# Optimization experiments

Measured on AMD Instinct MI355X. Metric: run time of the kernel, lower is better.

Reference implementation:

```python
import jax, jax.numpy as jnp
import numpy as np
from jax import lax

PART = 224   # PART_IMAGE_SIZE
PAD = 224    # PAD_SIZE
TOPN = 4
IOU_THRESH = 0.25
N_ANCHORS = 1614


def _conv(x, w, b, stride, pad):
    y = lax.conv_general_dilated(x, w, (stride, stride), [(pad, pad), (pad, pad)],
                                 dimension_numbers=('NCHW', 'OIHW', 'NCHW'))
    return y + b[None, :, None, None]


def _iou(box, boxes):
    # box [4], boxes [N,4] as (y0,x0,y1,x1)
    yy0 = jnp.maximum(box[0], boxes[:, 0]); xx0 = jnp.maximum(box[1], boxes[:, 1])
    yy1 = jnp.minimum(box[2], boxes[:, 2]); xx1 = jnp.minimum(box[3], boxes[:, 3])
    inter = jnp.clip(yy1 - yy0, 0.0) * jnp.clip(xx1 - xx0, 0.0)
    a = (box[2] - box[0]) * (box[3] - box[1])
    areas = (boxes[:, 2] - boxes[:, 0]) * (boxes[:, 3] - boxes[:, 1])
    return inter / (a + areas - inter)


def _nms(scores, boxes):
    # hard NMS keeping TOPN boxes; returns indices [TOPN]
    valid = jnp.ones(scores.shape, dtype=bool)
    idxs = []
    for _ in range(TOPN):
        i = jnp.argmax(jnp.where(valid, scores, -jnp.inf))
        idxs.append(i)
        valid = valid & (_iou(boxes[i], boxes) <= IOU_THRESH)
    return jnp.stack(idxs)


def _crop_resize(img, box):
    # img [3,Hp,Wp] padded image, box [4] float; bilinear, align_corners=True,
    # matching F.interpolate(x_pad[:, :, y0:y1, x0:x1], (PART, PART))
    Hp, Wp = img.shape[1], img.shape[2]
    def coords(c0, c1, L):
        t = jnp.arange(PART, dtype=img.dtype) / (PART - 1)
        c = c0 + (c1 - 1.0 - c0) * t          # absolute source coordinate
        cf = jnp.floor(c)
        lo = jnp.clip(cf.astype(jnp.int32), 0, L - 1)
        hi = jnp.clip(lo + 1, 0, L - 1)
        return lo, hi, c - cf
    yl, yh, wy = coords(box[0], box[2], Hp)
    xl, xh, wx = coords(box[1], box[3], Wp)
    g = lambda yi, xi: img[:, yi[:, None], xi[None, :]]   # [3,PART,PART]
    return ((1 - wy)[:, None] * ((1 - wx) * g(yl, xl) + wx * g(yl, xh))
            + wy[:, None] * ((1 - wx) * g(yh, xl) + wx * g(yh, xh)))


def setup_inputs() -> dict:
    key = jax.random.key(0)
    ks = jax.random.split(key, 20)
    x = jax.random.uniform(ks[0], (16, 3, 448, 448), dtype=jnp.float32)
    rpn_feature = jax.random.normal(ks[1], (16, 2048, 14, 14), dtype=jnp.float32)
    # valid boxes inside the padded 896x896 image
    y0 = jax.random.randint(ks[2], (N_ANCHORS,), 0, 560)
    x0 = jax.random.randint(ks[3], (N_ANCHORS,), 0, 560)
    h = jax.random.randint(ks[4], (N_ANCHORS,), 32, 336)
    w = jax.random.randint(ks[5], (N_ANCHORS,), 32, 336)
    anchors = jnp.stack([y0, x0, jnp.minimum(y0 + h, 896), jnp.minimum(x0 + w, 896)], axis=1).astype(jnp.int32)
    s = 0.02
    inp = {
        'x': x, 'rpn_feature': rpn_feature, 'anchors': anchors,
        'w_down1': jax.random.normal(ks[6], (128, 2048, 3, 3), jnp.float32) * s,
        'b_down1': jnp.zeros((128,), jnp.float32),
        'w_down2': jax.random.normal(ks[7], (128, 128, 3, 3), jnp.float32) * s,
        'b_down2': jnp.zeros((128,), jnp.float32),
        'w_down3': jax.random.normal(ks[8], (128, 128, 3, 3), jnp.float32) * s,
        'b_down3': jnp.zeros((128,), jnp.float32),
        'w_tidy1': jax.random.normal(ks[9], (6, 128, 1, 1), jnp.float32) * s,
        'b_tidy1': jnp.zeros((6,), jnp.float32),
        'w_tidy2': jax.random.normal(ks[10], (6, 128, 1, 1), jnp.float32) * s,
        'b_tidy2': jnp.zeros((6,), jnp.float32),
        'w_tidy3': jax.random.normal(ks[11], (9, 128, 1, 1), jnp.float32) * s,
        'b_tidy3': jnp.zeros((9,), jnp.float32),
    }
    return inp


def reference(x, rpn_feature, anchors,
              w_down1, b_down1, w_down2, b_down2, w_down3, b_down3,
              w_tidy1, b_tidy1, w_tidy2, b_tidy2, w_tidy3, b_tidy3):
    B = x.shape[0]
    # ProposalNet
    d1 = jax.nn.relu(_conv(rpn_feature, w_down1, b_down1, 1, 1))   # [B,128,14,14]
    d2 = jax.nn.relu(_conv(d1, w_down2, b_down2, 2, 1))            # [B,128,7,7]
    d3 = jax.nn.relu(_conv(d2, w_down3, b_down3, 2, 1))            # [B,128,4,4]
    t1 = _conv(d1, w_tidy1, b_tidy1, 1, 0).reshape(B, -1)
    t2 = _conv(d2, w_tidy2, b_tidy2, 1, 0).reshape(B, -1)
    t3 = _conv(d3, w_tidy3, b_tidy3, 1, 0).reshape(B, -1)
    rpn_score = jnp.concatenate([t1, t2, t3], axis=1)              # [B, 1614]
    boxes = anchors.astype(x.dtype)                                # [N,4]
    top_n_index = jax.vmap(lambda s: _nms(s, boxes))(rpn_score)    # [B,TOPN]
    top_n_prob = jnp.take_along_axis(rpn_score, top_n_index, axis=1)
    x_pad = jnp.pad(x, ((0, 0), (0, 0), (PAD, PAD), (PAD, PAD)))   # [B,3,896,896]
    sel_boxes = boxes[top_n_index]                                 # [B,TOPN,4]
    part_imgs = jax.vmap(lambda img, bxs: jax.vmap(lambda b: _crop_resize(img, b))(bxs))(x_pad, sel_boxes)
    # part_imgs: [B,TOPN,3,PART,PART]
    return rpn_score, top_n_index, top_n_prob, part_imgs
```

## Files before the change

kernel.cpp:

```cpp
#include <hip/hip_runtime.h>
#include <hip/hip_bf16.h>

#define NB 16
#define NA 1614

typedef __bf16 bf16x8 __attribute__((ext_vector_type(8)));
typedef float f32x4 __attribute__((ext_vector_type(4)));

__device__ __forceinline__ unsigned short f2bf(float v) {
  unsigned u = __float_as_uint(v);
  unsigned r = (u + 0x7FFFu + ((u >> 16) & 1u)) >> 16;
  return (unsigned short)r;
}
__device__ __forceinline__ float bf2f(unsigned short s) {
  return __uint_as_float(((unsigned)s) << 16);
}

__global__ void prep_w(const float* __restrict__ w, unsigned short* __restrict__ wTh,
                       unsigned short* __restrict__ wTl) {
  int e = blockIdx.x * 256 + threadIdx.x;
  if (e >= 9 * 128 * 2048) return;
  int tap = e / (128 * 2048);
  int rem = e - tap * (128 * 2048);
  int oc = rem >> 11, ic = rem & 2047;
  float v = w[((size_t)oc * 2048 + ic) * 9 + tap];
  unsigned short h = f2bf(v);
  wTh[e] = h;
  wTl[e] = f2bf(v - bf2f(h));
}

__global__ __launch_bounds__(256, 3)
void conv1_mfma(const float* __restrict__ in, const unsigned short* __restrict__ wTh,
                const unsigned short* __restrict__ wTl, float* __restrict__ pout,
                int atomic_mode) {
  const int bid = blockIdx.x;
  const int b  = bid & 15;
  const int nh = (bid >> 4) & 1;
  const int kc = bid >> 5;
  const int tid = threadIdx.x;
  const int wid = tid >> 6, lane = tid & 63;
  const int wm = wid & 1, wn = wid >> 1;
  const int q = lane >> 4, ln = lane & 15;

  __shared__ unsigned short sAh[256 * 40];
  __shared__ unsigned short sAl[256 * 40];
  __shared__ unsigned short sBh[64 * 40];
  __shared__ unsigned short sBl[64 * 40];

  for (int e = tid; e < 5120; e += 256) {
    ((unsigned int*)sAh)[e] = 0u;
    ((unsigned int*)sAl)[e] = 0u;
  }

  int abase[7];
#pragma unroll
  for (int mf = 0; mf < 7; mf++) {
    int row = wm * 112 + mf * 16 + ln;
    int y = row / 14, x = row - y * 14;
    abase[mf] = ((row < 196) ? (y * 16 + x) : 0) * 40 + q * 8;
  }

  f32x4 acc[7][2];
#pragma unroll
  for (int mf = 0; mf < 7; mf++)
#pragma unroll
    for (int nf = 0; nf < 2; nf++) acc[mf][nf] = (f32x4){0.f, 0.f, 0.f, 0.f};

  const float* inb = in + (size_t)b * 2048 * 196;

  const int boc = tid >> 2, bic0 = (tid & 3) * 8;
  const size_t bocbase = (size_t)(nh * 64 + boc) << 11;

  uint4 pvh, pvl;
  {
    size_t g = bocbase + kc * 128 + bic0;
    pvh = *(const uint4*)(wTh + g);
    pvl = *(const uint4*)(wTl + g);
  }

  for (int it = 0; it < 36; it++) {
    const int ks = it / 9, tap = it - ks * 9;
    const int icg0 = kc * 128 + ks * 32;
    __syncthreads();
    *(uint4*)(sBh + boc * 40 + bic0) = pvh;
    *(uint4*)(sBl + boc * 40 + bic0) = pvl;
    if (tap == 0) {
#pragma unroll
      for (int r = 0; r < 25; r++) {
        int e = tid + 256 * r;
        if (e < 6272) {
          int icl = e & 31, posl = e >> 5;
          float v = inb[(size_t)(icg0 + icl) * 196 + posl];
          unsigned short h = f2bf(v);
          unsigned short l = f2bf(v - bf2f(h));
          int py = posl / 14, px = posl - py * 14;
          int ad = ((py + 1) * 16 + px + 1) * 40 + icl;
          sAh[ad] = h;
          sAl[ad] = l;
        }
      }
    }
    {
      const int nit = (it < 35) ? it + 1 : 35;
      const int ks2 = nit / 9, tap2 = nit - ks2 * 9;
      size_t g = (size_t)tap2 * (128 * 2048) + bocbase + kc * 128 + ks2 * 32 + bic0;
      pvh = *(const uint4*)(wTh + g);
      pvl = *(const uint4*)(wTl + g);
    }
    __syncthreads();

    const int t40 = ((tap / 3) * 16 + (tap % 3)) * 40;
    bf16x8 bh[2], bl[2];
#pragma unroll
    for (int nf = 0; nf < 2; nf++) {
      const int bb = (wn * 32 + nf * 16 + ln) * 40 + q * 8;
      bh[nf] = *(const bf16x8*)(sBh + bb);
      bl[nf] = *(const bf16x8*)(sBl + bb);
    }
#pragma unroll
    for (int mf = 0; mf < 7; mf++) {
      bf16x8 ah = *(const bf16x8*)(sAh + abase[mf] + t40);
      bf16x8 al = *(const bf16x8*)(sAl + abase[mf] + t40);
#pragma unroll
      for (int nf = 0; nf < 2; nf++) {
        acc[mf][nf] = __builtin_amdgcn_mfma_f32_16x16x32_bf16(ah, bh[nf], acc[mf][nf], 0, 0, 0);
        acc[mf][nf] = __builtin_amdgcn_mfma_f32_16x16x32_bf16(al, bh[nf], acc[mf][nf], 0, 0, 0);
        acc[mf][nf] = __builtin_amdgcn_mfma_f32_16x16x32_bf16(ah, bl[nf], acc[mf][nf], 0, 0, 0);
      }
    }
  }

  if (atomic_mode) {
#pragma unroll
    for (int mf = 0; mf < 7; mf++) {
      const int row0 = wm * 112 + mf * 16 + q * 4;
#pragma unroll
      for (int nf = 0; nf < 2; nf++) {
        const int oc = nh * 64 + wn * 32 + nf * 16 + ln;
        float* dst = pout + ((size_t)b * 128 + oc) * 196;
#pragma unroll
        for (int r = 0; r < 4; r++) {
          const int row = row0 + r;
          if (row < 196) atomicAdd(dst + row, acc[mf][nf][r]);
        }
      }
    }
  } else {
    float* pk = pout + ((size_t)kc * NB + b) * 196 * 128;
#pragma unroll
    for (int mf = 0; mf < 7; mf++) {
      const int row0 = wm * 112 + mf * 16 + q * 4;
#pragma unroll
      for (int nf = 0; nf < 2; nf++) {
        const int oc = nh * 64 + wn * 32 + nf * 16 + ln;
#pragma unroll
        for (int r = 0; r < 4; r++) {
          const int row = row0 + r;
          if (row < 196) pk[(size_t)row * 128 + oc] = acc[mf][nf][r];
        }
      }
    }
  }
}

__global__ void conv1_finish_p(const float* __restrict__ p1, const float* __restrict__ bias,
                               float* __restrict__ d1) {
  const int i = blockIdx.x * 256 + threadIdx.x;
  if (i >= NB * 196 * 128) return;
  const int oc = i & 127;
  const int t = i >> 7;
  const int pos = t % 196, b = t / 196;
  float s = bias[oc];
#pragma unroll
  for (int k = 0; k < 16; k++) s += p1[(size_t)k * (NB * 196 * 128) + i];
  d1[((size_t)b * 128 + oc) * 196 + pos] = fmaxf(s, 0.f);
}

__global__ void conv1_finish_a(float* __restrict__ d1, const float* __restrict__ bias) {
  const int i = blockIdx.x * 256 + threadIdx.x;
  if (i >= NB * 128 * 196) return;
  const int oc = (i / 196) & 127;
  d1[i] = fmaxf(d1[i] + bias[oc], 0.f);
}

__global__ void conv2_part(const float* __restrict__ d1, const float* __restrict__ w,
                           float* __restrict__ p2) {
  const int bid = blockIdx.x;
  const int kc = bid & 3, oct = (bid >> 2) & 3, b = bid >> 4;
  const int ic0 = kc * 32, oc0 = oct * 32;
  const int tid = threadIdx.x;
  const int ocl = tid >> 3, rw = tid & 7;

  __shared__ float s_in[32 * 320];
  __shared__ float s_w[32 * 324];

#pragma unroll
  for (int r = 0; r < 32; r++) {
    const int e = tid + 256 * r;
    const int ch = e >> 8, idx = e & 255;
    const int tr = idx >> 4, tc = idx & 15;
    const int iy = tr - 1, ix = tc - 1;
    float v = 0.f;
    if ((unsigned)iy < 14u && (unsigned)ix < 14u)
      v = d1[((size_t)b * 128 + ic0 + ch) * 196 + iy * 14 + ix];
    s_in[ch * 320 + tr * 20 + tc] = v;
  }
#pragma unroll
  for (int r = 0; r < 36; r++) {
    const int e = tid + 256 * r;
    const int oc = e / 288, rem = e - oc * 288;
    const int ch = rem / 9, tap = rem - ch * 9;
    s_w[ch * 324 + tap * 36 + oc] =
        w[(size_t)(oc0 + oc) * 1152 + (size_t)ic0 * 9 + rem];
  }
  __syncthreads();

  if (rw < 7) {
    float acc[7] = {};
    for (int ic = 0; ic < 32; ic++) {
      const float* wrow = s_w + ic * 324 + ocl;
      const float* irow = s_in + ic * 320;
#pragma unroll
      for (int ky = 0; ky < 3; ky++) {
        const float* r = irow + (2 * rw + ky) * 20;
        const float4 f0 = *(const float4*)(r);
        const float4 f1 = *(const float4*)(r + 4);
        const float4 f2 = *(const float4*)(r + 8);
        const float4 f3 = *(const float4*)(r + 12);
        const float ev[8] = {f0.x, f0.z, f1.x, f1.z, f2.x, f2.z, f3.x, f3.z};
        const float od[7] = {f0.y, f0.w, f1.y, f1.w, f2.y, f2.w, f3.y};
        const float w0 = wrow[(ky * 3 + 0) * 36];
        const float w1 = wrow[(ky * 3 + 1) * 36];
        const float w2 = wrow[(ky * 3 + 2) * 36];
#pragma unroll
        for (int x = 0; x < 7; x++)
          acc[x] = fmaf(w0, ev[x], fmaf(w1, od[x], fmaf(w2, ev[x + 1], acc[x])));
      }
    }
    float* po = p2 + (((size_t)kc * NB + b) * 128 + oc0 + ocl) * 49 + rw * 7;
#pragma unroll
    for (int x = 0; x < 7; x++) po[x] = acc[x];
  }
}

__global__ void conv2_finish(const float* __restrict__ p2, const float* __restrict__ bias,
                             float* __restrict__ d2) {
  const int i = blockIdx.x * 256 + threadIdx.x;
  if (i >= NB * 128 * 49) return;
  const int oc = (i / 49) & 127;
  float s = bias[oc];
#pragma unroll
  for (int k = 0; k < 4; k++) s += p2[(size_t)k * (NB * 128 * 49) + i];
  d2[i] = fmaxf(s, 0.f);
}

__global__ void conv3_part(const float* __restrict__ d2, const float* __restrict__ w,
                           float* __restrict__ p3) {
  const int bid = blockIdx.x;
  const int kc = bid & 1, oct = (bid >> 1) & 7, b = bid >> 4;
  const int ic0 = kc * 64, oc0 = oct * 16;
  const int tid = threadIdx.x;
  const int oc = tid >> 4, p = tid & 15;
  const int y = p >> 2, x = p & 3;

  __shared__ float s_in[64 * 108];
  __shared__ float s_w[64 * 144];

#pragma unroll
  for (int r = 0; r < 21; r++) {
    const int e = tid + 256 * r;
    if (e < 64 * 81) {
      const int ch = e / 81, idx = e - ch * 81;
      const int tr = idx / 9, tc = idx - tr * 9;
      const int iy = tr - 1, ix = tc - 1;
      float v = 0.f;
      if ((unsigned)iy < 7u && (unsigned)ix < 7u)
        v = d2[((size_t)b * 128 + ic0 + ch) * 49 + iy * 7 + ix];
      s_in[ch * 108 + tr * 12 + tc] = v;
    }
  }
#pragma unroll
  for (int r = 0; r < 36; r++) {
    const int e = tid + 256 * r;
    const int o = e / 576, rem = e - o * 576;
    const int ch = rem / 9, tap = rem - ch * 9;
    s_w[ch * 144 + tap * 16 + o] =
        w[(size_t)(oc0 + o) * 1152 + (size_t)ic0 * 9 + rem];
  }
  __syncthreads();

  float acc = 0.f;
  for (int ic = 0; ic < 64; ic++) {
    const float* wrow = s_w + ic * 144 + oc;
    const float* irow = s_in + ic * 108 + 2 * y * 12 + 2 * x;
#pragma unroll
    for (int ky = 0; ky < 3; ky++)
#pragma unroll
      for (int kx = 0; kx < 3; kx++)
        acc = fmaf(wrow[(ky * 3 + kx) * 16], irow[ky * 12 + kx], acc);
  }
  p3[(((size_t)kc * NB + b) * 128 + oc0 + oc) * 16 + p] = acc;
}

__global__ void conv3_finish(const float* __restrict__ p3, const float* __restrict__ bias,
                             float* __restrict__ d3) {
  const int i = blockIdx.x * 256 + threadIdx.x;
  if (i >= NB * 128 * 16) return;
  const int oc = (i >> 4) & 127;
  float s = bias[oc] + p3[i] + p3[(size_t)(NB * 128 * 16) + i];
  d3[i] = fmaxf(s, 0.f);
}

__global__ void tidy_kernel(const float* __restrict__ d1, const float* __restrict__ d2,
                            const float* __restrict__ d3,
                            const float* __restrict__ w1, const float* __restrict__ b1,
                            const float* __restrict__ w2, const float* __restrict__ b2,
                            const float* __restrict__ w3, const float* __restrict__ b3,
                            float* __restrict__ score) {
  int i = blockIdx.x * 256 + threadIdx.x;
  if (i >= NB * NA) return;
  int b = i / NA, j = i - b * NA;
  float s;
  if (j < 1176) {
    int oc = j / 196, p = j - oc * 196;
    const float* in = d1 + (size_t)b * 128 * 196 + p;
    const float* w = w1 + oc * 128;
    s = b1[oc];
#pragma unroll 8
    for (int ic = 0; ic < 128; ic++) s += in[(size_t)ic * 196] * w[ic];
  } else if (j < 1470) {
    int jj = j - 1176;
    int oc = jj / 49, p = jj - oc * 49;
    const float* in = d2 + (size_t)b * 128 * 49 + p;
    const float* w = w2 + oc * 128;
    s = b2[oc];
#pragma unroll 8
    for (int ic = 0; ic < 128; ic++) s += in[(size_t)ic * 49] * w[ic];
  } else {
    int jj = j - 1470;
    int oc = jj / 16, p = jj & 15;
    const float* in = d3 + (size_t)b * 128 * 16 + p;
    const float* w = w3 + oc * 128;
    s = b3[oc];
#pragma unroll 8
    for (int ic = 0; ic < 128; ic++) s += in[(size_t)ic * 16] * w[ic];
  }
  score[i] = s;
}

__global__ void nms_kernel(const float* __restrict__ score, const int* __restrict__ anchors,
                           float* __restrict__ out_idx, float* __restrict__ out_prob,
                           float* __restrict__ sel) {
  __shared__ float s_sc[NA];
  __shared__ float s_bx[NA * 4];
  __shared__ float r_s[256];
  __shared__ int r_i[256];
  const int b = blockIdx.x, tid = threadIdx.x;

  for (int i = tid; i < NA; i += 256) {
    s_sc[i] = score[b * NA + i];
    s_bx[i * 4 + 0] = (float)anchors[i * 4 + 0];
    s_bx[i * 4 + 1] = (float)anchors[i * 4 + 1];
    s_bx[i * 4 + 2] = (float)anchors[i * 4 + 2];
    s_bx[i * 4 + 3] = (float)anchors[i * 4 + 3];
  }
  __syncthreads();

  for (int t = 0; t < 4; t++) {
    float bs = -__builtin_inff();
    int bi = NA;
    for (int i = tid; i < NA; i += 256) {
      float s = s_sc[i];
      if (s > bs || (s == bs && i < bi)) { bs = s; bi = i; }
    }
    r_s[tid] = bs; r_i[tid] = bi;
    __syncthreads();
    for (int off = 128; off > 0; off >>= 1) {
      if (tid < off) {
        float s2 = r_s[tid + off]; int i2 = r_i[tid + off];
        if (s2 > r_s[tid] || (s2 == r_s[tid] && i2 < r_i[tid])) { r_s[tid] = s2; r_i[tid] = i2; }
      }
      __syncthreads();
    }
    const int idx = r_i[0];
    const float by0 = s_bx[idx * 4 + 0], bx0 = s_bx[idx * 4 + 1];
    const float by1 = s_bx[idx * 4 + 2], bx1 = s_bx[idx * 4 + 3];
    if (tid == 0) {
      out_idx[b * 4 + t] = (float)idx;
      out_prob[b * 4 + t] = s_sc[idx];
      sel[(b * 4 + t) * 4 + 0] = by0;
      sel[(b * 4 + t) * 4 + 1] = bx0;
      sel[(b * 4 + t) * 4 + 2] = by1;
      sel[(b * 4 + t) * 4 + 3] = bx1;
    }
    __syncthreads();
    const float a = (by1 - by0) * (bx1 - bx0);
    for (int i = tid; i < NA; i += 256) {
      float cy0 = s_bx[i * 4 + 0], cx0 = s_bx[i * 4 + 1];
      float cy1 = s_bx[i * 4 + 2], cx1 = s_bx[i * 4 + 3];
      float yy0 = fmaxf(by0, cy0), xx0 = fmaxf(bx0, cx0);
      float yy1 = fminf(by1, cy1), xx1 = fminf(bx1, cx1);
      float inter = fmaxf(yy1 - yy0, 0.f) * fmaxf(xx1 - xx0, 0.f);
      float ar = (cy1 - cy0) * (cx1 - cx0);
      float iou = inter / (a + ar - inter);
      if (iou > 0.25f) s_sc[i] = -__builtin_inff();
    }
    __syncthreads();
  }
}

__global__ void crop_kernel(const float* __restrict__ x, const float* __restrict__ sel,
                            float* __restrict__ out) {
  long long i = (long long)blockIdx.x * 256 + threadIdx.x;
  const long long total = (long long)NB * 4 * 3 * 224 * 224;
  if (i >= total) return;
  int px = (int)(i % 224);
  long long t = i / 224;
  int py = (int)(t % 224); t /= 224;
  int ch = (int)(t % 3);  t /= 3;
  int n  = (int)(t % 4);
  int b  = (int)(t / 4);

  const float* bx = sel + (b * 4 + n) * 4;
  const float y0 = bx[0], x0 = bx[1], y1 = bx[2], x1 = bx[3];

  float ty = (float)py / 223.0f;
  float cy = y0 + (y1 - 1.0f - y0) * ty;
  float cyf = floorf(cy);
  int ylo = (int)cyf; ylo = ylo < 0 ? 0 : (ylo > 895 ? 895 : ylo);
  int yhi = ylo + 1 > 895 ? 895 : ylo + 1;
  float wy = cy - cyf;

  float tx = (float)px / 223.0f;
  float cx = x0 + (x1 - 1.0f - x0) * tx;
  float cxf = floorf(cx);
  int xlo = (int)cxf; xlo = xlo < 0 ? 0 : (xlo > 895 ? 895 : xlo);
  int xhi = xlo + 1 > 895 ? 895 : xlo + 1;
  float wx = cx - cxf;

  const float* img = x + ((size_t)b * 3 + ch) * 448 * 448;
  auto g = [&](int yy, int xx) -> float {
    yy -= 224; xx -= 224;
    if ((unsigned)yy < 448u && (unsigned)xx < 448u)
      return img[(size_t)yy * 448 + xx];
    return 0.f;
  };
  float v00 = g(ylo, xlo), v01 = g(ylo, xhi);
  float v10 = g(yhi, xlo), v11 = g(yhi, xhi);
  float r = (1.f - wy) * ((1.f - wx) * v00 + wx * v01) +
            wy * ((1.f - wx) * v10 + wx * v11);
  out[i] = r;
}

extern "C" void kernel_launch(void* const* d_in, const int* in_sizes, int n_in,
                              void* d_out, int out_size, void* d_ws, size_t ws_size,
                              hipStream_t stream) {
  const float* x    = (const float*)d_in[0];
  const float* rpn  = (const float*)d_in[1];
  const int*   anc  = (const int*)d_in[2];
  const float* w_d1 = (const float*)d_in[3];
  const float* b_d1 = (const float*)d_in[4];
  const float* w_d2 = (const float*)d_in[5];
  const float* b_d2 = (const float*)d_in[6];
  const float* w_d3 = (const float*)d_in[7];
  const float* b_d3 = (const float*)d_in[8];
  const float* w_t1 = (const float*)d_in[9];
  const float* b_t1 = (const float*)d_in[10];
  const float* w_t2 = (const float*)d_in[11];
  const float* b_t2 = (const float*)d_in[12];
  const float* w_t3 = (const float*)d_in[13];
  const float* b_t3 = (const float*)d_in[14];

  float* out = (float*)d_out;
  float* ws = (float*)d_ws;

  float* d1  = ws;
  float* d2  = d1 + 401408;
  float* d3  = d2 + 100352;
  float* sel = d3 + 32768;
  float* p2  = sel + 256;
  float* p3  = p2 + 401408;
  unsigned short* wTh = (unsigned short*)(p3 + 65536);
  unsigned short* wTl = wTh + 2359296;
  float* p1  = (float*)(wTl + 2359296);

  const size_t need_partials =
      (size_t)(401408 + 100352 + 32768 + 256 + 401408 + 65536 + 6422528) * 4 +
      (size_t)2 * 2359296 * 2;
  const int atomic_mode = (ws_size >= need_partials) ? 0 : 1;

  float* score    = out;
  float* out_idx  = out + 25824;
  float* out_prob = out + 25888;
  float* parts    = out + 25952;

  prep_w<<<dim3(9216), dim3(256), 0, stream>>>(w_d1, wTh, wTl);
  if (atomic_mode) {
    hipMemsetAsync(d1, 0, (size_t)NB * 128 * 196 * sizeof(float), stream);
    conv1_mfma<<<dim3(512), dim3(256), 0, stream>>>(rpn, wTh, wTl, d1, 1);
    conv1_finish_a<<<dim3(1568), dim3(256), 0, stream>>>(d1, b_d1);
  } else {
    conv1_mfma<<<dim3(512), dim3(256), 0, stream>>>(rpn, wTh, wTl, p1, 0);
    conv1_finish_p<<<dim3(1568), dim3(256), 0, stream>>>(p1, b_d1, d1);
  }
  conv2_part<<<dim3(256), dim3(256), 0, stream>>>(d1, w_d2, p2);
  conv2_finish<<<dim3(392), dim3(256), 0, stream>>>(p2, b_d2, d2);
  conv3_part<<<dim3(256), dim3(256), 0, stream>>>(d2, w_d3, p3);
  conv3_finish<<<dim3(128), dim3(256), 0, stream>>>(p3, b_d3, d3);
  tidy_kernel<<<dim3(101), dim3(256), 0, stream>>>(d1, d2, d3, w_t1, b_t1, w_t2, b_t2,
                                                   w_t3, b_t3, score);
  nms_kernel<<<dim3(16), dim3(256), 0, stream>>>(score, anc, out_idx, out_prob, sel);
  crop_kernel<<<dim3(37632), dim3(256), 0, stream>>>(x, sel, parts);
}
```

Before: 306.7 us.

## Pre-split conv1 activations to bf16 hi/lo layout and fuse tidy scoring into NMS

A new prep_a kernel converts the rpn feature map once into hi/lo bf16 arrays laid out position-major with 32-channel groups, so conv1 can fill its LDS tile with vector copies instead of scattered scalar loads and per-element conversions. The atomic fallback path is dropped, and conv1 partials now go into the output's part-image region as scratch, which crop_kernel later overwrites. The tidy 1x1 convs and NMS are fused into one 16-block kernel that stages weights and inputs in shared memory, removing a launch and a global round trip of the scores. Costs are an extra kernel pass over the activations, and the fused scoring runs on only 16 blocks.

Result: faster. 299.6 us (-2.3%).

```diff
diff --git a/kernel.cpp b/kernel.cpp
--- a/kernel.cpp
+++ b/kernel.cpp
@@ -29,10 +29,48 @@
   wTl[e] = f2bf(v - bf2f(h));
 }
 
+__global__ __launch_bounds__(256)
+void prep_a(const float* __restrict__ in, unsigned short* __restrict__ aTh,
+            unsigned short* __restrict__ aTl) {
+  const int bid = blockIdx.x;
+  const int chunk = bid & 63, b = bid >> 6;
+  __shared__ float s[32 * 200];
+  const float* src = in + ((size_t)b * 2048 + chunk * 32) * 196;
+#pragma unroll
+  for (int r = 0; r < 7; r++) {
+    int e = threadIdx.x + 256 * r;
+    if (e < 1568) {
+      int ic = e / 49, f = e - ic * 49;
+      float4 v = ((const float4*)(src + (size_t)ic * 196))[f];
+      *(float4*)(s + ic * 200 + f * 4) = v;
+    }
+  }
+  __syncthreads();
+  unsigned short* oh = aTh + (size_t)bid * 196 * 32;
+  unsigned short* ol = aTl + (size_t)bid * 196 * 32;
+#pragma unroll
+  for (int r = 0; r < 4; r++) {
+    int e = threadIdx.x + 256 * r;
+    if (e < 784) {
+      int g = e / 196, pos = e - g * 196;
+      unsigned short hv[8], lv[8];
+#pragma unroll
+      for (int j = 0; j < 8; j++) {
+        float v = s[(g * 8 + j) * 200 + pos];
+        unsigned short h = f2bf(v);
+        hv[j] = h;
+        lv[j] = f2bf(v - bf2f(h));
+      }
+      *(uint4*)(oh + (size_t)pos * 32 + g * 8) = *(uint4*)hv;
+      *(uint4*)(ol + (size_t)pos * 32 + g * 8) = *(uint4*)lv;
+    }
+  }
+}
+
 __global__ __launch_bounds__(256, 3)
-void conv1_mfma(const float* __restrict__ in, const unsigned short* __restrict__ wTh,
-                const unsigned short* __restrict__ wTl, float* __restrict__ pout,
-                int atomic_mode) {
+void conv1_mfma(const unsigned short* __restrict__ aTh, const unsigned short* __restrict__ aTl,
+                const unsigned short* __restrict__ wTh, const unsigned short* __restrict__ wTl,
+                float* __restrict__ p1) {
   const int bid = blockIdx.x;
   const int b  = bid & 15;
   const int nh = (bid >> 4) & 1;
@@ -66,8 +104,6 @@
 #pragma unroll
     for (int nf = 0; nf < 2; nf++) acc[mf][nf] = (f32x4){0.f, 0.f, 0.f, 0.f};
 
-  const float* inb = in + (size_t)b * 2048 * 196;
-
   const int boc = tid >> 2, bic0 = (tid & 3) * 8;
   const size_t bocbase = (size_t)(nh * 64 + boc) << 11;
 
@@ -80,23 +116,21 @@
 
   for (int it = 0; it < 36; it++) {
     const int ks = it / 9, tap = it - ks * 9;
-    const int icg0 = kc * 128 + ks * 32;
     __syncthreads();
     *(uint4*)(sBh + boc * 40 + bic0) = pvh;
     *(uint4*)(sBl + boc * 40 + bic0) = pvl;
     if (tap == 0) {
-#pragma unroll
-      for (int r = 0; r < 25; r++) {
+      const uint4* gh = (const uint4*)(aTh + ((size_t)(b * 64 + kc * 4 + ks) * 196) * 32);
+      const uint4* gl = (const uint4*)(aTl + ((size_t)(b * 64 + kc * 4 + ks) * 196) * 32);
+#pragma unroll
+      for (int r = 0; r < 4; r++) {
         int e = tid + 256 * r;
-        if (e < 6272) {
-          int icl = e & 31, posl = e >> 5;
-          float v = inb[(size_t)(icg0 + icl) * 196 + posl];
-          unsigned short h = f2bf(v);
-          unsigned short l = f2bf(v - bf2f(h));
-          int py = posl / 14, px = posl - py * 14;
-          int ad = ((py + 1) * 16 + px + 1) * 40 + icl;
-          sAh[ad] = h;
-          sAl[ad] = l;
+        if (e < 784) {
+          int slot = e >> 2, part = e & 3;
+          int py = slot / 14, px = slot - py * 14;
+          int dst = ((py + 1) * 16 + px + 1) * 40 + part * 8;
+          *(uint4*)(sAh + dst) = gh[e];
+          *(uint4*)(sAl + dst) = gl[e];
         }
       }
     }
@@ -130,34 +164,17 @@
     }
   }
 
-  if (atomic_mode) {
-#pragma unroll
-    for (int mf = 0; mf < 7; mf++) {
-      const int row0 = wm * 112 + mf * 16 + q * 4;
-#pragma unroll
-      for (int nf = 0; nf < 2; nf++) {
-        const int oc = nh * 64 + wn * 32 + nf * 16 + ln;
-        float* dst = pout + ((size_t)b * 128 + oc) * 196;
-#pragma unroll
-        for (int r = 0; r < 4; r++) {
-          const int row = row0 + r;
-          if (row < 196) atomicAdd(dst + row, acc[mf][nf][r]);
-        }
-      }
-    }
-  } else {
-    float* pk = pout + ((size_t)kc * NB + b) * 196 * 128;
-#pragma unroll
-    for (int mf = 0; mf < 7; mf++) {
-      const int row0 = wm * 112 + mf * 16 + q * 4;
-#pragma unroll
-      for (int nf = 0; nf < 2; nf++) {
-        const int oc = nh * 64 + wn * 32 + nf * 16 + ln;
-#pragma unroll
-        for (int r = 0; r < 4; r++) {
-          const int row = row0 + r;
-          if (row < 196) pk[(size_t)row * 128 + oc] = acc[mf][nf][r];
-        }
+  float* pk = p1 + ((size_t)kc * NB + b) * 196 * 128;
+#pragma unroll
+  for (int mf = 0; mf < 7; mf++) {
+    const int row0 = wm * 112 + mf * 16 + q * 4;
+#pragma unroll
+    for (int nf = 0; nf < 2; nf++) {
+      const int oc = nh * 64 + wn * 32 + nf * 16 + ln;
+#pragma unroll
+      for (int r = 0; r < 4; r++) {
+        const int row = row0 + r;
+        if (row < 196) pk[(size_t)row * 128 + oc] = acc[mf][nf][r];
       }
     }
   }
@@ -174,13 +191,6 @@
 #pragma unroll
   for (int k = 0; k < 16; k++) s += p1[(size_t)k * (NB * 196 * 128) + i];
   d1[((size_t)b * 128 + oc) * 196 + pos] = fmaxf(s, 0.f);
-}
-
-__global__ void conv1_finish_a(float* __restrict__ d1, const float* __restrict__ bias) {
-  const int i = blockIdx.x * 256 + threadIdx.x;
-  if (i >= NB * 128 * 196) return;
-  const int oc = (i / 196) & 127;
-  d1[i] = fmaxf(d1[i] + bias[oc], 0.f);
 }
 
 __global__ void conv2_part(const float* __restrict__ d1, const float* __restrict__ w,
@@ -311,58 +321,114 @@
   d3[i] = fmaxf(s, 0.f);
 }
 
-__global__ void tidy_kernel(const float* __restrict__ d1, const float* __restrict__ d2,
-                            const float* __restrict__ d3,
-                            const float* __restrict__ w1, const float* __restrict__ b1,
-                            const float* __restrict__ w2, const float* __restrict__ b2,
-                            const float* __restrict__ w3, const float* __restrict__ b3,
-                            float* __restrict__ score) {
-  int i = blockIdx.x * 256 + threadIdx.x;
-  if (i >= NB * NA) return;
-  int b = i / NA, j = i - b * NA;
-  float s;
-  if (j < 1176) {
-    int oc = j / 196, p = j - oc * 196;
-    const float* in = d1 + (size_t)b * 128 * 196 + p;
-    const float* w = w1 + oc * 128;
-    s = b1[oc];
-#pragma unroll 8
-    for (int ic = 0; ic < 128; ic++) s += in[(size_t)ic * 196] * w[ic];
-  } else if (j < 1470) {
-    int jj = j - 1176;
-    int oc = jj / 49, p = jj - oc * 49;
-    const float* in = d2 + (size_t)b * 128 * 49 + p;
-    const float* w = w2 + oc * 128;
-    s = b2[oc];
-#pragma unroll 8
-    for (int ic = 0; ic < 128; ic++) s += in[(size_t)ic * 49] * w[ic];
-  } else {
-    int jj = j - 1470;
-    int oc = jj / 16, p = jj & 15;
-    const float* in = d3 + (size_t)b * 128 * 16 + p;
-    const float* w = w3 + oc * 128;
-    s = b3[oc];
-#pragma unroll 8
-    for (int ic = 0; ic < 128; ic++) s += in[(size_t)ic * 16] * w[ic];
-  }
-  score[i] = s;
-}
-
-__global__ void nms_kernel(const float* __restrict__ score, const int* __restrict__ anchors,
-                           float* __restrict__ out_idx, float* __restrict__ out_prob,
-                           float* __restrict__ sel) {
+__global__ __launch_bounds__(256, 1)
+void score_nms(const float* __restrict__ d1, const float* __restrict__ d2,
+               const float* __restrict__ d3,
+               const float* __restrict__ w1, const float* __restrict__ b1,
+               const float* __restrict__ w2, const float* __restrict__ b2,
+               const float* __restrict__ w3, const float* __restrict__ b3,
+               const int* __restrict__ anchors, float* __restrict__ score,
+               float* __restrict__ out_idx, float* __restrict__ out_prob,
+               float* __restrict__ sel) {
+  __shared__ float s_in[32 * 200];
+  __shared__ float s_w[21 * 128];
+  __shared__ float s_b[21];
   __shared__ float s_sc[NA];
   __shared__ float s_bx[NA * 4];
   __shared__ float r_s[256];
   __shared__ int r_i[256];
   const int b = blockIdx.x, tid = threadIdx.x;
 
+  for (int i = tid; i < 768; i += 256) s_w[i] = w1[i];
+  for (int i = tid; i < 768; i += 256) s_w[768 + i] = w2[i];
+  for (int i = tid; i < 1152; i += 256) s_w[1536 + i] = w3[i];
+  if (tid < 21) s_b[tid] = (tid < 6) ? b1[tid] : (tid < 12) ? b2[tid - 6] : b3[tid - 12];
   for (int i = tid; i < NA; i += 256) {
-    s_sc[i] = score[b * NA + i];
     s_bx[i * 4 + 0] = (float)anchors[i * 4 + 0];
     s_bx[i * 4 + 1] = (float)anchors[i * 4 + 1];
     s_bx[i * 4 + 2] = (float)anchors[i * 4 + 2];
     s_bx[i * 4 + 3] = (float)anchors[i * 4 + 3];
+  }
+
+  float acc[5] = {0.f, 0.f, 0.f, 0.f, 0.f};
+  for (int chunk = 0; chunk < 4; chunk++) {
+    __syncthreads();
+    const float* src = d1 + ((size_t)b * 128 + chunk * 32) * 196;
+#pragma unroll
+    for (int r = 0; r < 7; r++) {
+      int e = tid + 256 * r;
+      if (e < 1568) {
+        int ic = e / 49, f = e - ic * 49;
+        *(float4*)(s_in + ic * 200 + f * 4) = ((const float4*)(src + (size_t)ic * 196))[f];
+      }
+    }
+    __syncthreads();
+#pragma unroll
+    for (int k = 0; k < 5; k++) {
+      int j = tid + 256 * k;
+      if (j < 1176) {
+        int oc = j / 196, p = j - oc * 196;
+        const float* wr = s_w + oc * 128 + chunk * 32;
+        float s = acc[k];
+#pragma unroll
+        for (int ic = 0; ic < 32; ic++) s = fmaf(wr[ic], s_in[ic * 200 + p], s);
+        acc[k] = s;
+      }
+    }
+  }
+#pragma unroll
+  for (int k = 0; k < 5; k++) {
+    int j = tid + 256 * k;
+    if (j < 1176) {
+      int oc = j / 196;
+      float s = acc[k] + s_b[oc];
+      s_sc[j] = s;
+      score[b * NA + j] = s;
+    }
+  }
+
+  __syncthreads();
+  {
+    const float* src = d2 + (size_t)b * 6272;
+#pragma unroll
+    for (int r = 0; r < 7; r++) {
+      int e = tid + 256 * r;
+      if (e < 1568) *(float4*)(s_in + e * 4) = ((const float4*)src)[e];
+    }
+  }
+  __syncthreads();
+#pragma unroll
+  for (int k = 0; k < 2; k++) {
+    int jj = tid + 256 * k;
+    if (jj < 294) {
+      int oc = jj / 49, p = jj - oc * 49;
+      const float* wr = s_w + 768 + oc * 128;
+      float s = s_b[6 + oc];
+#pragma unroll 8
+      for (int ic = 0; ic < 128; ic++) s = fmaf(wr[ic], s_in[ic * 49 + p], s);
+      s_sc[1176 + jj] = s;
+      score[b * NA + 1176 + jj] = s;
+    }
+  }
+
+  __syncthreads();
+  {
+    const float* src = d3 + (size_t)b * 2048;
+#pragma unroll
+    for (int r = 0; r < 2; r++) {
+      int e = tid + 256 * r;
+      if (e < 512) *(float4*)(s_in + e * 4) = ((const float4*)src)[e];
+    }
+  }
+  __syncthreads();
+  if (tid < 144) {
+    int oc = tid >> 4, p = tid & 15;
+    const float* wr = s_w + 1536 + oc * 128;
+    float s = s_b[12 + oc];
+#pragma unroll 8
+    for (int ic = 0; ic < 128; ic++) s = fmaf(wr[ic], s_in[ic * 16 + p], s);
+    s_sc[1470 + tid] = s;
+    score[b * NA + 1470 + tid] = s;
   }
   __syncthreads();
 
@@ -482,33 +548,24 @@
   float* p3  = p2 + 401408;
   unsigned short* wTh = (unsigned short*)(p3 + 65536);
   unsigned short* wTl = wTh + 2359296;
-  float* p1  = (float*)(wTl + 2359296);
-
-  const size_t need_partials =
-      (size_t)(401408 + 100352 + 32768 + 256 + 401408 + 65536 + 6422528) * 4 +
-      (size_t)2 * 2359296 * 2;
-  const int atomic_mode = (ws_size >= need_partials) ? 0 : 1;
+  unsigned short* aTh = wTl + 2359296;
+  unsigned short* aTl = aTh + 6422528;
 
   float* score    = out;
   float* out_idx  = out + 25824;
   float* out_prob = out + 25888;
   float* parts    = out + 25952;
+  float* p1       = parts;
 
   prep_w<<<dim3(9216), dim3(256), 0, stream>>>(w_d1, wTh, wTl);
-  if (atomic_mode) {
-    hipMemsetAsync(d1, 0, (size_t)NB * 128 * 196 * sizeof(float), stream);
-    conv1_mfma<<<dim3(512), dim3(256), 0, stream>>>(rpn, wTh, wTl, d1, 1);
-    conv1_finish_a<<<dim3(1568), dim3(256), 0, stream>>>(d1, b_d1);
-  } else {
-    conv1_mfma<<<dim3(512), dim3(256), 0, stream>>>(rpn, wTh, wTl, p1, 0);
-    conv1_finish_p<<<dim3(1568), dim3(256), 0, stream>>>(p1, b_d1, d1);
-  }
+  prep_a<<<dim3(1024), dim3(256), 0, stream>>>(rpn, aTh, aTl);
+  conv1_mfma<<<dim3(512), dim3(256), 0, stream>>>(aTh, aTl, wTh, wTl, p1);
+  conv1_finish_p<<<dim3(1568), dim3(256), 0, stream>>>(p1, b_d1, d1);
   conv2_part<<<dim3(256), dim3(256), 0, stream>>>(d1, w_d2, p2);
   conv2_finish<<<dim3(392), dim3(256), 0, stream>>>(p2, b_d2, d2);
   conv3_part<<<dim3(256), dim3(256), 0, stream>>>(d2, w_d3, p3);
   conv3_finish<<<dim3(128), dim3(256), 0, stream>>>(p3, b_d3, d3);
-  tidy_kernel<<<dim3(101), dim3(256), 0, stream>>>(d1, d2, d3, w_t1, b_t1, w_t2, b_t2,
-                                                   w_t3, b_t3, score);
-  nms_kernel<<<dim3(16), dim3(256), 0, stream>>>(score, anc, out_idx, out_prob, sel);
+  score_nms<<<dim3(16), dim3(256), 0, stream>>>(d1, d2, d3, w_t1, b_t1, w_t2, b_t2,
+                                                w_t3, b_t3, anc, score, out_idx, out_prob, sel);
   crop_kernel<<<dim3(37632), dim3(256), 0, stream>>>(x, sel, parts);
 }
```
